# Kernel optimization log

Measured on AMD Instinct MI355X. Metric: run time of the kernel, lower is better.

## Reference

```python
import jax, jax.numpy as jnp
import numpy as np

B, C, N, M, H = 2, 512, 2048, 2048, 8
HD = C // H
SCALE = HD ** -0.5


def setup_inputs() -> dict:
    key = jax.random.key(0)
    ks = jax.random.split(key, 8)
    x = jax.random.normal(ks[0], (B, C, N), dtype=jnp.float32)
    y = jax.random.normal(ks[1], (B, C, M), dtype=jnp.float32)
    # linear weights stored as [in, out] so out = in @ W (equivalent to torch Linear)
    Wq = jax.random.normal(ks[2], (C, C), dtype=jnp.float32) * (C ** -0.5)
    Wkv = jax.random.normal(ks[3], (C, 2 * C), dtype=jnp.float32) * (C ** -0.5)
    # depthwise Conv1d, kernel_size=1, groups=C -> per-channel scale + bias
    lw = jax.random.normal(ks[4], (C,), dtype=jnp.float32)
    lb = jax.random.normal(ks[5], (C,), dtype=jnp.float32) * 0.01
    Wp = jax.random.normal(ks[6], (C, C), dtype=jnp.float32) * (C ** -0.5)
    bp = jax.random.normal(ks[7], (C,), dtype=jnp.float32) * 0.01
    return {"x": x, "y": y, "Wq": Wq, "Wkv": Wkv, "lw": lw, "lb": lb, "Wp": Wp, "bp": bp}


def reference(x, y, Wq, Wkv, lw, lb, Wp, bp):
    # x: [B,C,N], y: [B,C,M]
    q = (x.transpose(0, 2, 1) @ Wq).reshape(B, N, H, HD).transpose(0, 2, 1, 3)  # [B,H,N,HD]
    kv = (y.transpose(0, 2, 1) @ Wkv).reshape(B, M, H, HD, 2).transpose(0, 2, 1, 3, 4)
    k, v = kv[..., 0], kv[..., 1]  # [B,H,M,HD]
    attn = jax.nn.softmax(jnp.einsum('bhnd,bhmd->bhnm', q, k) * SCALE, axis=-1)
    # depthwise conv1d (ksize=1) on v laid out as [B,C,M]; channel c = h*HD + d
    lw2 = lw.reshape(H, HD)[None, :, None, :]
    lb2 = lb.reshape(H, HD)[None, :, None, :]
    v = v + v * lw2 + lb2
    out = jnp.einsum('bhnm,bhmd->bhnd', attn, v).transpose(0, 2, 1, 3).reshape(B, N, C)
    out = (out @ Wp + bp).transpose(0, 2, 1)  # [B,C,N]
    return out
```

## Files before the change

### kernel.cpp

```cpp
#include <hip/hip_runtime.h>

#define Bb 2
#define Cc 512
#define Nn 2048
#define Mm 2048
#define Hh 8
#define HD 64
#define QSCALE 0.18033688011112042f

typedef unsigned short u16;
typedef unsigned int u32;
typedef __bf16 bf16x8 __attribute__((ext_vector_type(8)));
typedef float f32x16 __attribute__((ext_vector_type(16)));

union V4 {
    uint4 u;
    bf16x8 b;
};

__device__ __forceinline__ u16 f2bfu(float f) {
    unsigned int b = __float_as_uint(f);
    unsigned int r = (b + 0x7fffu + ((b >> 16) & 1u)) >> 16;
    return (u16)r;
}
__device__ __forceinline__ u32 pkbf(float lo, float hi_) {
    return __builtin_amdgcn_perm(__float_as_uint(hi_) + 0x8000u,
                                 __float_as_uint(lo) + 0x8000u, 0x07060302u);
}

__global__ __launch_bounds__(256) void transpose_all(
    const float* __restrict__ x, const float* __restrict__ y, const float* __restrict__ Wq,
    const float* __restrict__ Wkv, const float* __restrict__ Wp, u16* __restrict__ xT,
    u16* __restrict__ yT, u16* __restrict__ WqT, u16* __restrict__ WkvT,
    u16* __restrict__ WpT) {
    __shared__ float tile[32][33];
    const int z = blockIdx.z;
    const float* in;
    u16* out;
    int S, sx = blockIdx.x;
    size_t base = 0;
    const int R = 512;
    if (z < 4) {
        in = (z < 2) ? x : y;
        out = (z < 2) ? xT : yT;
        S = 2048;
        base = (size_t)(z & 1) * R * S;
    } else {
        if (sx < 16) {
            in = Wq; out = WqT; S = 512;
        } else if (sx < 48) {
            in = Wkv; out = WkvT; S = 1024; sx -= 16;
        } else {
            in = Wp; out = WpT; S = 512; sx -= 48;
        }
    }
    int r0 = blockIdx.y * 32, s0 = sx * 32;
    int tx = threadIdx.x, ty = threadIdx.y;
#pragma unroll
    for (int k = 0; k < 4; k++)
        tile[ty + 8 * k][tx] = in[base + (size_t)(r0 + ty + 8 * k) * S + s0 + tx];
    __syncthreads();
#pragma unroll
    for (int k = 0; k < 4; k++)
        out[base + (size_t)(s0 + ty + 8 * k) * R + r0 + tx] = f2bfu(tile[tx][ty + 8 * k]);
}

__global__ __launch_bounds__(256) void proj_qkv(const u16* __restrict__ xT,
                                                const u16* __restrict__ yT,
                                                const u16* __restrict__ WqT,
                                                const u16* __restrict__ WkvT,
                                                const float* __restrict__ lw,
                                                const float* __restrict__ lb,
                                                u16* __restrict__ qb, u16* __restrict__ kb,
                                                u16* __restrict__ vtb) {
    __shared__ alignas(16) u16 As[2][128 * 64];
    __shared__ alignas(16) u16 Bs[2][64 * 64];
    const int t = threadIdx.x;
    const int lane = t & 63, w = t >> 6;
    const int r = lane & 31, hi = lane >> 5;
    const bool isQ = (blockIdx.x < 8);
    const int c0 = (isQ ? blockIdx.x : blockIdx.x - 8) * 64;
    const int r0 = blockIdx.y * 128;
    const int wr = (w & 1) * 64, wc = (w >> 1) * 32;
    const u16* A = isQ ? xT : yT;
    const u16* Bt = isQ ? WqT : WkvT;

    const int sra = t >> 3, ska = t & 7;
    const int swa = ((ska ^ (sra & 7)) << 3);
    const u16* Ag = A + (size_t)(r0 + sra) * 512 + ska * 8;
    const u16* Bg = Bt + (size_t)(c0 + sra) * 512 + ska * 8;

    {
#pragma unroll
        for (int i = 0; i < 4; i++)
            *(uint4*)&As[0][(sra + 32 * i) * 64 + swa] = *(const uint4*)(Ag + (size_t)i * 32 * 512);
#pragma unroll
        for (int i = 0; i < 2; i++)
            *(uint4*)&Bs[0][(sra + 32 * i) * 64 + swa] = *(const uint4*)(Bg + (size_t)i * 32 * 512);
    }
    __syncthreads();

    f32x16 acc[2];
#pragma unroll
    for (int rs = 0; rs < 2; rs++)
#pragma unroll
        for (int e = 0; e < 16; e++) acc[rs][e] = 0.f;

    const int ra0 = wr + r, ra1 = wr + 32 + r, rb = wc + r;

    for (int kk = 0; kk < 8; kk++) {
        const int cur = kk & 1;
        uint4 pa[4], pb[2];
        const bool more = (kk < 7);
        if (more) {
            const size_t ko = (size_t)(kk + 1) * 64;
#pragma unroll
            for (int i = 0; i < 4; i++) pa[i] = *(const uint4*)(Ag + (size_t)i * 32 * 512 + ko);
#pragma unroll
            for (int i = 0; i < 2; i++) pb[i] = *(const uint4*)(Bg + (size_t)i * 32 * 512 + ko);
        }
        V4 af[2][4], bf[4];
#pragma unroll
        for (int ks = 0; ks < 4; ks++) {
            const int c = 2 * ks + hi;
            bf[ks].u = *(const uint4*)&Bs[cur][rb * 64 + ((c ^ (rb & 7)) << 3)];
            af[0][ks].u = *(const uint4*)&As[cur][ra0 * 64 + ((c ^ (ra0 & 7)) << 3)];
            af[1][ks].u = *(const uint4*)&As[cur][ra1 * 64 + ((c ^ (ra1 & 7)) << 3)];
        }
#pragma unroll
        for (int ks = 0; ks < 4; ks++) {
            acc[0] = __builtin_amdgcn_mfma_f32_32x32x16_bf16(af[0][ks].b, bf[ks].b, acc[0], 0, 0, 0);
            acc[1] = __builtin_amdgcn_mfma_f32_32x32x16_bf16(af[1][ks].b, bf[ks].b, acc[1], 0, 0, 0);
        }
        if (more) {
            const int nxt = cur ^ 1;
#pragma unroll
            for (int i = 0; i < 4; i++) *(uint4*)&As[nxt][(sra + 32 * i) * 64 + swa] = pa[i];
#pragma unroll
            for (int i = 0; i < 2; i++) *(uint4*)&Bs[nxt][(sra + 32 * i) * 64 + swa] = pb[i];
        }
        __syncthreads();
    }

    const int cg = c0 + wc + r;
    if (isQ) {
#pragma unroll
        for (int rs = 0; rs < 2; rs++)
#pragma unroll
            for (int e = 0; e < 16; e++) {
                int m = r0 + wr + rs * 32 + 4 * hi + (e & 3) + 8 * (e >> 2);
                qb[(size_t)m * 512 + cg] = f2bfu(acc[rs][e] * QSCALE);
            }
    } else {
        const int hd = cg >> 1, s = cg & 1, h = hd >> 6, d = hd & 63;
        const int bq = r0 >> 11;
        const int bh = bq * 8 + h;
        const int mb = (r0 & 2047) + wr + 4 * hi;
        if (s == 0) {
            u16* kbase = kb + ((size_t)bh * 2048) * 64 + d;
#pragma unroll
            for (int rs = 0; rs < 2; rs++)
#pragma unroll
                for (int e = 0; e < 16; e++) {
                    int m = mb + rs * 32 + (e & 3) + 8 * (e >> 2);
                    kbase[(size_t)m * 64] = f2bfu(acc[rs][e]);
                }
        } else {
            const float sw = 1.0f + lw[hd], sb = lb[hd];
            u16* vbase = vtb + ((size_t)bh * 64 + d) * 2048;
#pragma unroll
            for (int rs = 0; rs < 2; rs++)
#pragma unroll
                for (int eg = 0; eg < 4; eg++) {
                    int m = mb + rs * 32 + 8 * eg;
                    float v0 = acc[rs][4 * eg + 0] * sw + sb;
                    float v1 = acc[rs][4 * eg + 1] * sw + sb;
                    float v2 = acc[rs][4 * eg + 2] * sw + sb;
                    float v3 = acc[rs][4 * eg + 3] * sw + sb;
                    uint2 pk;
                    pk.x = pkbf(v0, v1);
                    pk.y = pkbf(v2, v3);
                    *(uint2*)(vbase + m) = pk;
                }
        }
    }
}

__global__ __launch_bounds__(256, 2) void flash_attn(const u16* __restrict__ q,
                                                     const u16* __restrict__ kk,
                                                     const u16* __restrict__ vt,
                                                     float* __restrict__ po,
                                                     float* __restrict__ ls) {
    __shared__ alignas(16) u16 Ks[2][64 * 64];
    __shared__ alignas(16) u16 Vs[2][64 * 64];
    const int t = threadIdx.x;
    const int lane = t & 63, w = t >> 6;
    const int r = lane & 31, hi = lane >> 5;
    const int nt = blockIdx.x & 7, sp = blockIdx.x >> 3;
    const int h = blockIdx.y, b = blockIdx.z;
    const int bh = b * Hh + h;
    const int nw0 = nt * 256 + 64 * w + r;
    const int MT0 = sp * 8, MT1 = MT0 + 8;

    V4 qf[2][4];
    {
        const u16* qrow = q + ((size_t)(b * Nn + nw0)) * Cc + h * HD + hi * 8;
#pragma unroll
        for (int ks = 0; ks < 4; ks++) {
            qf[0][ks].u = *(const uint4*)(qrow + ks * 16);
            qf[1][ks].u = *(const uint4*)(qrow + 32 * Cc + ks * 16);
        }
    }

    const u16* kbase = kk + ((size_t)bh) * Mm * HD;
    const u16* vbase = vt + ((size_t)bh) * HD * Mm;

    const int cr0 = t >> 3, cc0 = t & 7;
    const int cr1 = cr0 + 32, cc1 = cc0;
    const int swa0 = cr0 * 64 + ((cc0 ^ (cr0 & 7)) << 3);
    const int swa1 = cr1 * 64 + ((cc1 ^ (cr1 & 7)) << 3);

    {
        int m00 = MT0 * 64;
        uint4 a0 = *(const uint4*)(kbase + (size_t)(m00 + cr0) * HD + cc0 * 8);
        uint4 a1 = *(const uint4*)(kbase + (size_t)(m00 + cr1) * HD + cc1 * 8);
        uint4 b0 = *(const uint4*)(vbase + (size_t)cr0 * Mm + m00 + cc0 * 8);
        uint4 b1 = *(const uint4*)(vbase + (size_t)cr1 * Mm + m00 + cc1 * 8);
        *(uint4*)&Ks[0][swa0] = a0;
        *(uint4*)&Ks[0][swa1] = a1;
        *(uint4*)&Vs[0][swa0] = b0;
        *(uint4*)&Vs[0][swa1] = b1;
    }
    __syncthreads();

    f32x16 oa[2][2];
#pragma unroll
    for (int v = 0; v < 2; v++)
#pragma unroll
        for (int nh = 0; nh < 2; nh++)
#pragma unroll
            for (int e = 0; e < 16; e++) oa[v][nh][e] = 0.f;
    float lsum0 = 0.f, lsum1 = 0.f;

    for (int mt = MT0; mt < MT1; mt++) {
        const int cur = mt & 1;
        uint4 nk0, nk1, nv0, nv1;
        const bool more = (mt + 1 < MT1);
        if (more) {
            int m0 = (mt + 1) * 64;
            nk0 = *(const uint4*)(kbase + (size_t)(m0 + cr0) * HD + cc0 * 8);
            nk1 = *(const uint4*)(kbase + (size_t)(m0 + cr1) * HD + cc1 * 8);
            nv0 = *(const uint4*)(vbase + (size_t)cr0 * Mm + m0 + cc0 * 8);
            nv1 = *(const uint4*)(vbase + (size_t)cr1 * Mm + m0 + cc1 * 8);
        }
        f32x16 sa[2][2];
#pragma unroll
        for (int s = 0; s < 2; s++) {
#pragma unroll
            for (int nh = 0; nh < 2; nh++)
#pragma unroll
                for (int e = 0; e < 16; e++) sa[s][nh][e] = 0.f;
#pragma unroll
            for (int ks = 0; ks < 4; ks++) {
                V4 af;
                af.u = *(const uint4*)&Ks[cur][(32 * s + r) * 64 +
                                               (((2 * ks + hi) ^ (r & 7)) << 3)];
                sa[s][0] = __builtin_amdgcn_mfma_f32_32x32x16_bf16(af.b, qf[0][ks].b,
                                                                   sa[s][0], 0, 0, 0);
                sa[s][1] = __builtin_amdgcn_mfma_f32_32x32x16_bf16(af.b, qf[1][ks].b,
                                                                   sa[s][1], 0, 0, 0);
            }
        }
#pragma unroll
        for (int s = 0; s < 2; s++) {
            u32 p[2][8];
#pragma unroll
            for (int qq = 0; qq < 8; qq++) {
                float e0 = __builtin_amdgcn_exp2f(sa[s][0][2 * qq]);
                float e1 = __builtin_amdgcn_exp2f(sa[s][0][2 * qq + 1]);
                lsum0 += e0 + e1;
                p[0][qq] = pkbf(e0, e1);
                float f0 = __builtin_amdgcn_exp2f(sa[s][1][2 * qq]);
                float f1 = __builtin_amdgcn_exp2f(sa[s][1][2 * qq + 1]);
                lsum1 += f0 + f1;
                p[1][qq] = pkbf(f0, f1);
            }
            u32 xr[2][4];
#pragma unroll
            for (int nh = 0; nh < 2; nh++) {
                xr[nh][0] = __shfl_xor(hi ? p[nh][0] : p[nh][2], 32);
                xr[nh][1] = __shfl_xor(hi ? p[nh][1] : p[nh][3], 32);
                xr[nh][2] = __shfl_xor(hi ? p[nh][4] : p[nh][6], 32);
                xr[nh][3] = __shfl_xor(hi ? p[nh][5] : p[nh][7], 32);
            }
#pragma unroll
            for (int kl = 0; kl < 2; kl++) {
                V4 pf[2];
#pragma unroll
                for (int nh = 0; nh < 2; nh++) {
                    if (kl == 0) {
                        pf[nh].u.x = hi ? xr[nh][0] : p[nh][0];
                        pf[nh].u.y = hi ? xr[nh][1] : p[nh][1];
                        pf[nh].u.z = hi ? p[nh][2] : xr[nh][0];
                        pf[nh].u.w = hi ? p[nh][3] : xr[nh][1];
                    } else {
                        pf[nh].u.x = hi ? xr[nh][2] : p[nh][4];
                        pf[nh].u.y = hi ? xr[nh][3] : p[nh][5];
                        pf[nh].u.z = hi ? p[nh][6] : xr[nh][2];
                        pf[nh].u.w = hi ? p[nh][7] : xr[nh][3];
                    }
                }
                const int c = 4 * s + 2 * kl + hi;
                V4 vf0, vf1;
                vf0.u = *(const uint4*)&Vs[cur][r * 64 + ((c ^ (r & 7)) << 3)];
                vf1.u = *(const uint4*)&Vs[cur][(32 + r) * 64 + ((c ^ (r & 7)) << 3)];
                oa[0][0] = __builtin_amdgcn_mfma_f32_32x32x16_bf16(vf0.b, pf[0].b, oa[0][0], 0, 0, 0);
                oa[0][1] = __builtin_amdgcn_mfma_f32_32x32x16_bf16(vf0.b, pf[1].b, oa[0][1], 0, 0, 0);
                oa[1][0] = __builtin_amdgcn_mfma_f32_32x32x16_bf16(vf1.b, pf[0].b, oa[1][0], 0, 0, 0);
                oa[1][1] = __builtin_amdgcn_mfma_f32_32x32x16_bf16(vf1.b, pf[1].b, oa[1][1], 0, 0, 0);
            }
        }
        if (more) {
            const int nxt = cur ^ 1;
            *(uint4*)&Ks[nxt][swa0] = nk0;
            *(uint4*)&Ks[nxt][swa1] = nk1;
            *(uint4*)&Vs[nxt][swa0] = nv0;
            *(uint4*)&Vs[nxt][swa1] = nv1;
        }
        __syncthreads();
    }

    lsum0 += __shfl_xor(lsum0, 32);
    lsum1 += __shfl_xor(lsum1, 32);
    float* pob = po + (((size_t)sp * 16 + bh) * 64) * 2048 + nw0;
#pragma unroll
    for (int e = 0; e < 16; e++) {
        int d0 = (e & 3) + 8 * (e >> 2) + 4 * hi;
        pob[(size_t)d0 * 2048] = oa[0][0][e];
        pob[(size_t)(d0 + 32) * 2048] = oa[1][0][e];
        pob[(size_t)d0 * 2048 + 32] = oa[0][1][e];
        pob[(size_t)(d0 + 32) * 2048 + 32] = oa[1][1][e];
    }
    if (hi == 0) {
        ls[((size_t)sp * 16 + bh) * 2048 + nw0] = lsum0;
        ls[((size_t)sp * 16 + bh) * 2048 + nw0 + 32] = lsum1;
    }
}

__global__ __launch_bounds__(256) void combine_o(const float* __restrict__ po,
                                                 const float* __restrict__ ls,
                                                 u16* __restrict__ o) {
    __shared__ u16 tile[64][72];
    const int t = threadIdx.x;
    const int n0 = blockIdx.x * 64, bh = blockIdx.y;
    const int n = n0 + (t & 63), dg = t >> 6;
    float linv;
    {
        float s = 0.f;
#pragma unroll
        for (int sp = 0; sp < 4; sp++) s += ls[((size_t)sp * 16 + bh) * 2048 + n];
        linv = 1.0f / s;
    }
#pragma unroll
    for (int i = 0; i < 16; i++) {
        int d = dg * 16 + i;
        float acc = 0.f;
#pragma unroll
        for (int sp = 0; sp < 4; sp++)
            acc += po[(((size_t)sp * 16 + bh) * 64 + d) * 2048 + n];
        tile[t & 63][d] = f2bfu(acc * linv);
    }
    __syncthreads();
    const int nr = t >> 2, dq = (t & 3) * 16;
    const int b = bh >> 3, h = bh & 7;
    u16* orow = o + ((size_t)(b * Nn + n0 + nr)) * Cc + h * 64 + dq;
    *(uint4*)(orow + 0) = *(const uint4*)&tile[nr][dq];
    *(uint4*)(orow + 8) = *(const uint4*)&tile[nr][dq + 8];
}

__global__ __launch_bounds__(256) void gemm_out(const u16* __restrict__ Wt,
                                                const u16* __restrict__ Ob,
                                                float* __restrict__ out,
                                                const float* __restrict__ bias) {
    __shared__ alignas(16) u16 Ws[2][64 * 64];
    __shared__ alignas(16) u16 Os[2][128 * 64];
    const int t = threadIdx.x;
    const int lane = t & 63, w = t >> 6;
    const int r = lane & 31, hi = lane >> 5;
    const int c0 = blockIdx.x * 64, n0 = blockIdx.y * 128;
    const int cb = (w & 1) * 32, nb = (w >> 1) * 32;

    const int sra = t >> 3, ska = t & 7;
    const int swa = ((ska ^ (sra & 7)) << 3);
    const u16* Wg = Wt + (size_t)(c0 + sra) * 512 + ska * 8;
    const u16* Og = Ob + (size_t)(n0 + sra) * 512 + ska * 8;

    {
#pragma unroll
        for (int i = 0; i < 2; i++)
            *(uint4*)&Ws[0][(sra + 32 * i) * 64 + swa] = *(const uint4*)(Wg + (size_t)i * 32 * 512);
#pragma unroll
        for (int i = 0; i < 4; i++)
            *(uint4*)&Os[0][(sra + 32 * i) * 64 + swa] = *(const uint4*)(Og + (size_t)i * 32 * 512);
    }
    __syncthreads();

    f32x16 acc[2];
#pragma unroll
    for (int ns = 0; ns < 2; ns++)
#pragma unroll
        for (int e = 0; e < 16; e++) acc[ns][e] = 0.f;

    const int rw = cb + r, ro0 = nb + r, ro1 = nb + 64 + r;

    for (int kk = 0; kk < 8; kk++) {
        const int cur = kk & 1;
        uint4 pw[2], po_[4];
        const bool more = (kk < 7);
        if (more) {
            const size_t ko = (size_t)(kk + 1) * 64;
#pragma unroll
            for (int i = 0; i < 2; i++) pw[i] = *(const uint4*)(Wg + (size_t)i * 32 * 512 + ko);
#pragma unroll
            for (int i = 0; i < 4; i++) po_[i] = *(const uint4*)(Og + (size_t)i * 32 * 512 + ko);
        }
        V4 wf[4], of[2][4];
#pragma unroll
        for (int ks = 0; ks < 4; ks++) {
            const int c = 2 * ks + hi;
            wf[ks].u = *(const uint4*)&Ws[cur][rw * 64 + ((c ^ (rw & 7)) << 3)];
            of[0][ks].u = *(const uint4*)&Os[cur][ro0 * 64 + ((c ^ (ro0 & 7)) << 3)];
            of[1][ks].u = *(const uint4*)&Os[cur][ro1 * 64 + ((c ^ (ro1 & 7)) << 3)];
        }
#pragma unroll
        for (int ks = 0; ks < 4; ks++) {
            acc[0] = __builtin_amdgcn_mfma_f32_32x32x16_bf16(wf[ks].b, of[0][ks].b, acc[0], 0, 0, 0);
            acc[1] = __builtin_amdgcn_mfma_f32_32x32x16_bf16(wf[ks].b, of[1][ks].b, acc[1], 0, 0, 0);
        }
        if (more) {
            const int nxt = cur ^ 1;
#pragma unroll
            for (int i = 0; i < 2; i++) *(uint4*)&Ws[nxt][(sra + 32 * i) * 64 + swa] = pw[i];
#pragma unroll
            for (int i = 0; i < 4; i++) *(uint4*)&Os[nxt][(sra + 32 * i) * 64 + swa] = po_[i];
        }
        __syncthreads();
    }

#pragma unroll
    for (int e = 0; e < 16; e++) {
        const int c_r = c0 + cb + 4 * hi + (e & 3) + 8 * (e >> 2);
        const float bv = bias[c_r];
#pragma unroll
        for (int ns = 0; ns < 2; ns++) {
            const int rg = n0 + nb + ns * 64 + r;
            const int b = rg >> 11, n = rg & 2047;
            out[((size_t)b * 512 + c_r) * 2048 + n] = acc[ns][e] + bv;
        }
    }
}

static const size_t OFF_XT = 0;
static const size_t OFF_YT = 4194304;
static const size_t OFF_WQT = 8388608;
static const size_t OFF_WKVT = 8912896;
static const size_t OFF_WPT = 9961472;
static const size_t OFF_Q = 10485760;
static const size_t OFF_K = 23068672;
static const size_t OFF_VT = 27262976;
static const size_t OFF_O = 31457280;
static const size_t OFF_PO = 35651584;
static const size_t OFF_LS = 69206016;

extern "C" void kernel_launch(void* const* d_in, const int* in_sizes, int n_in,
                              void* d_out, int out_size, void* d_ws, size_t ws_size,
                              hipStream_t stream) {
    const float* x = (const float*)d_in[0];
    const float* y = (const float*)d_in[1];
    const float* Wq = (const float*)d_in[2];
    const float* Wkv = (const float*)d_in[3];
    const float* lw = (const float*)d_in[4];
    const float* lb = (const float*)d_in[5];
    const float* Wp = (const float*)d_in[6];
    const float* bp = (const float*)d_in[7];

    char* ws = (char*)d_ws;
    u16* xT = (u16*)(ws + OFF_XT);
    u16* yT = (u16*)(ws + OFF_YT);
    u16* WqT = (u16*)(ws + OFF_WQT);
    u16* WkvT = (u16*)(ws + OFF_WKVT);
    u16* WpT = (u16*)(ws + OFF_WPT);
    u16* qb = (u16*)(ws + OFF_Q);
    u16* kb = (u16*)(ws + OFF_K);
    u16* vtb = (u16*)(ws + OFF_VT);
    u16* ob = (u16*)(ws + OFF_O);
    float* po = (float*)(ws + OFF_PO);
    float* lsw = (float*)(ws + OFF_LS);

    dim3 tb(32, 8, 1);
    transpose_all<<<dim3(64, 16, 5), tb, 0, stream>>>(x, y, Wq, Wkv, Wp, xT, yT, WqT, WkvT,
                                                      WpT);
    proj_qkv<<<dim3(24, 32), 256, 0, stream>>>(xT, yT, WqT, WkvT, lw, lb, qb, kb, vtb);
    flash_attn<<<dim3(32, Hh, Bb), 256, 0, stream>>>(qb, kb, vtb, po, lsw);
    combine_o<<<dim3(Nn / 64, Bb * Hh), 256, 0, stream>>>(po, lsw, ob);
    gemm_out<<<dim3(8, 32), 256, 0, stream>>>(WpT, ob, (float*)d_out, bp);
}
```

Measured before the change: 138.0 us.

## Store split-K attention partials as bf16 and remap blocks for XCD locality

The flash attention partial outputs are now written as bf16 instead of fp32, which halves the write traffic and the combine kernel's read traffic. The launch grid is flattened to 1D and block ids are remapped so that blocks sharing the same (bh, split) K/V range land on the same XCD, to improve L2 reuse. The partials lose precision before the split reduction, which could add rounding error.

```diff
diff --git a/kernel.cpp b/kernel.cpp
--- a/kernel.cpp
+++ b/kernel.cpp
@@ -22,6 +22,9 @@
     unsigned int b = __float_as_uint(f);
     unsigned int r = (b + 0x7fffu + ((b >> 16) & 1u)) >> 16;
     return (u16)r;
+}
+__device__ __forceinline__ float bfu2f(u16 u) {
+    return __uint_as_float(((unsigned int)u) << 16);
 }
 __device__ __forceinline__ u32 pkbf(float lo, float hi_) {
     return __builtin_amdgcn_perm(__float_as_uint(hi_) + 0x8000u,
@@ -189,16 +192,19 @@
 __global__ __launch_bounds__(256, 2) void flash_attn(const u16* __restrict__ q,
                                                      const u16* __restrict__ kk,
                                                      const u16* __restrict__ vt,
-                                                     float* __restrict__ po,
+                                                     u16* __restrict__ po,
                                                      float* __restrict__ ls) {
     __shared__ alignas(16) u16 Ks[2][64 * 64];
     __shared__ alignas(16) u16 Vs[2][64 * 64];
     const int t = threadIdx.x;
     const int lane = t & 63, w = t >> 6;
     const int r = lane & 31, hi = lane >> 5;
-    const int nt = blockIdx.x & 7, sp = blockIdx.x >> 3;
-    const int h = blockIdx.y, b = blockIdx.z;
-    const int bh = b * Hh + h;
+    const int id = blockIdx.x;
+    const int xcd = id & 7, sid = id >> 3;
+    const int combo = xcd * 8 + (sid >> 3);
+    const int nt = sid & 7;
+    const int bh = combo >> 2, sp = combo & 3;
+    const int b = bh >> 3, h = bh & 7;
     const int nw0 = nt * 256 + 64 * w + r;
     const int MT0 = sp * 8, MT1 = MT0 + 8;
 
@@ -332,14 +338,14 @@
 
     lsum0 += __shfl_xor(lsum0, 32);
     lsum1 += __shfl_xor(lsum1, 32);
-    float* pob = po + (((size_t)sp * 16 + bh) * 64) * 2048 + nw0;
+    u16* pob = po + (((size_t)sp * 16 + bh) * 64) * 2048 + nw0;
 #pragma unroll
     for (int e = 0; e < 16; e++) {
         int d0 = (e & 3) + 8 * (e >> 2) + 4 * hi;
-        pob[(size_t)d0 * 2048] = oa[0][0][e];
-        pob[(size_t)(d0 + 32) * 2048] = oa[1][0][e];
-        pob[(size_t)d0 * 2048 + 32] = oa[0][1][e];
-        pob[(size_t)(d0 + 32) * 2048 + 32] = oa[1][1][e];
+        pob[(size_t)d0 * 2048] = f2bfu(oa[0][0][e]);
+        pob[(size_t)(d0 + 32) * 2048] = f2bfu(oa[1][0][e]);
+        pob[(size_t)d0 * 2048 + 32] = f2bfu(oa[0][1][e]);
+        pob[(size_t)(d0 + 32) * 2048 + 32] = f2bfu(oa[1][1][e]);
     }
     if (hi == 0) {
         ls[((size_t)sp * 16 + bh) * 2048 + nw0] = lsum0;
@@ -347,7 +353,7 @@
     }
 }
 
-__global__ __launch_bounds__(256) void combine_o(const float* __restrict__ po,
+__global__ __launch_bounds__(256) void combine_o(const u16* __restrict__ po,
                                                  const float* __restrict__ ls,
                                                  u16* __restrict__ o) {
     __shared__ u16 tile[64][72];
@@ -367,7 +373,7 @@
         float acc = 0.f;
 #pragma unroll
         for (int sp = 0; sp < 4; sp++)
-            acc += po[(((size_t)sp * 16 + bh) * 64 + d) * 2048 + n];
+            acc += bfu2f(po[(((size_t)sp * 16 + bh) * 64 + d) * 2048 + n]);
         tile[t & 63][d] = f2bfu(acc * linv);
     }
     __syncthreads();
@@ -494,14 +500,14 @@
     u16* kb = (u16*)(ws + OFF_K);
     u16* vtb = (u16*)(ws + OFF_VT);
     u16* ob = (u16*)(ws + OFF_O);
-    float* po = (float*)(ws + OFF_PO);
+    u16* po = (u16*)(ws + OFF_PO);
     float* lsw = (float*)(ws + OFF_LS);
 
     dim3 tb(32, 8, 1);
     transpose_all<<<dim3(64, 16, 5), tb, 0, stream>>>(x, y, Wq, Wkv, Wp, xT, yT, WqT, WkvT,
                                                       WpT);
     proj_qkv<<<dim3(24, 32), 256, 0, stream>>>(xT, yT, WqT, WkvT, lw, lb, qb, kb, vtb);
-    flash_attn<<<dim3(32, Hh, Bb), 256, 0, stream>>>(qb, kb, vtb, po, lsw);
+    flash_attn<<<dim3(512), 256, 0, stream>>>(qb, kb, vtb, po, lsw);
     combine_o<<<dim3(Nn / 64, Bb * Hh), 256, 0, stream>>>(po, lsw, ob);
     gemm_out<<<dim3(8, 32), 256, 0, stream>>>(WpT, ob, (float*)d_out, bp);
 }
```

Result: faster. 135.1 us (-2.1%).
